# Kernel optimization log

Hardware: AMD Instinct MI355X
Metric: run time of the kernel (lower is better)

Reference implementation:

```python
import jax, jax.numpy as jnp
import numpy as np

EPS = 1e-8  # torch.nn.CosineSimilarity default eps


def setup_inputs() -> dict:
    key = jax.random.key(0)
    k1, k2 = jax.random.split(key)
    B, D = 2048, 512
    return {
        "z_i": jax.random.normal(k1, (B, D), dtype=jnp.float32),
        "z_j": jax.random.normal(k2, (B, D), dtype=jnp.float32),
        "temperature": 0.5,
    }


def _neg_mask_indices(B):
    # static (numpy) mask: remove diagonal and the two +/-B positive diagonals
    N = 2 * B
    mask = np.ones((N, N), dtype=bool)
    np.fill_diagonal(mask, False)
    idx = np.arange(B)
    mask[idx, idx + B] = False
    mask[idx + B, idx] = False
    rows, cols = np.where(mask)  # each row keeps exactly N-2 entries, row-major order
    return rows, cols


def reference(z_i, z_j, temperature):
    B = z_i.shape[0]
    N = 2 * B
    z = jnp.concatenate([z_i, z_j], axis=0)                      # [N, D]
    # cosine similarity = normalized GEMM (same math as pairwise CosineSimilarity)
    zn = z / jnp.maximum(jnp.linalg.norm(z, axis=1, keepdims=True), EPS)
    sim = jnp.matmul(zn, zn.T) / temperature                      # [N, N]

    pos = jnp.concatenate([jnp.diagonal(sim, B), jnp.diagonal(sim, -B)])[:, None]  # [N, 1]
    rows, cols = _neg_mask_indices(B)
    neg = sim[rows, cols].reshape(N, N - 2)                       # [N, N-2]

    logits = jnp.concatenate([pos, neg], axis=1)                  # [N, N-1], label = 0
    # sum-reduced cross-entropy with label 0, divided by N
    loss = jnp.sum(jax.nn.logsumexp(logits, axis=1) - logits[:, 0]) / N

    # avg_rank: position of the positive (column 0) in descending sort of logits
    order = jnp.argsort(-logits, axis=1)
    avg_rank = jnp.mean(jnp.argmin(order, axis=1).astype(jnp.float32))
    return loss, avg_rank
```

## Files before the change

### kernel.cpp

```cpp
#include <hip/hip_runtime.h>
#include <math.h>

#define DDIM 512
#define THREADS 128
#define BT 64
#define NT 64
#define NTILES (NT * (NT + 1) / 2)
#define NSL 16
#define NCH 64

typedef __attribute__((ext_vector_type(8))) __bf16 bf16x8;
typedef __attribute__((ext_vector_type(4))) float f32x4;
typedef __attribute__((ext_vector_type(8))) unsigned short ushort8;

__device__ __forceinline__ float bf2f(unsigned short u) {
  union { unsigned int i; float f; } v; v.i = ((unsigned int)u) << 16; return v.f;
}
__device__ __forceinline__ unsigned short f2bf(float f) {
  unsigned int u = __builtin_bit_cast(unsigned int, f);
  return (unsigned short)((u + 0x7fffu + ((u >> 16) & 1u)) >> 16);
}

__device__ __forceinline__ size_t frag_off_us(int rt, int s, int lane) {
  return ((size_t)(rt * NSL + s) * 64 + lane) * 8;
}

__global__ void k_prep(const float* __restrict__ zi, const float* __restrict__ zj,
                       const float* __restrict__ tempp,
                       unsigned short* __restrict__ zf, float* __restrict__ pos,
                       int B) {
  int wv = (blockIdx.x * blockDim.x + threadIdx.x) >> 6;
  int lane = threadIdx.x & 63;
  if (wv >= B) return;
  const float* a = zi + (size_t)wv * DDIM;
  const float* b = zj + (size_t)wv * DDIM;
  float4 a0 = *(const float4*)(a + lane * 8);
  float4 a1 = *(const float4*)(a + lane * 8 + 4);
  float4 b0 = *(const float4*)(b + lane * 8);
  float4 b1 = *(const float4*)(b + lane * 8 + 4);
  float av[8] = {a0.x, a0.y, a0.z, a0.w, a1.x, a1.y, a1.z, a1.w};
  float bv[8] = {b0.x, b0.y, b0.z, b0.w, b1.x, b1.y, b1.z, b1.w};
  float sa = 0.f, sb = 0.f;
#pragma unroll
  for (int i = 0; i < 8; ++i) { sa = fmaf(av[i], av[i], sa); sb = fmaf(bv[i], bv[i], sb); }
#pragma unroll
  for (int off = 32; off; off >>= 1) { sa += __shfl_xor(sa, off, 64); sb += __shfl_xor(sb, off, 64); }
  float ia = 1.f / fmaxf(sqrtf(sa), 1e-8f);
  float ib = 1.f / fmaxf(sqrtf(sb), 1e-8f);
  ushort8 ua, ub;
  float fa[8], fb[8];
#pragma unroll
  for (int i = 0; i < 8; ++i) {
    unsigned short x = f2bf(av[i] * ia); ua[i] = x; fa[i] = bf2f(x);
    unsigned short y = f2bf(bv[i] * ib); ub[i] = y; fb[i] = bf2f(y);
  }
  const int s = lane >> 2, g = lane & 3;
  {
    int r = wv;
    *(ushort8*)(zf + frag_off_us(r >> 4, s, (g << 4) | (r & 15))) = ua;
    r = wv + B;
    *(ushort8*)(zf + frag_off_us(r >> 4, s, (g << 4) | (r & 15))) = ub;
  }
  float pd = 0.f;
#pragma unroll
  for (int i = 0; i < 8; ++i) pd = fmaf(fa[i], fb[i], pd);
#pragma unroll
  for (int off = 32; off; off >>= 1) pd += __shfl_xor(pd, off, 64);
  if (lane == 0) {
    float p = pd / tempp[0];
    pos[wv] = p; pos[wv + B] = p;
  }
}

__global__ __launch_bounds__(THREADS) void k_main(
    const unsigned short* __restrict__ zf, const float* __restrict__ pos,
    const float* __restrict__ tempp, float* __restrict__ partS,
    float* __restrict__ partC, int B) {
  int tri = (blockIdx.x & 7) * (NTILES / 8) + (blockIdx.x >> 3);
  int bi = 0;
  while (tri >= NT - bi) { tri -= NT - bi; ++bi; }
  const int bj = bi + tri;
  const int r0 = bi * BT, c0 = bj * BT;
  const bool diag = (bi == bj);
  const float invt = 1.0f / tempp[0];

  const int t = threadIdx.x;
  const int lane = t & 63;
  const int wave = t >> 6;
  const int cl = lane & 15, g = lane >> 4;

  const int art0 = (r0 >> 4) + wave * 2;
  const int brt0 = (c0 >> 4);

  f32x4 acc[2][4];
#pragma unroll
  for (int m = 0; m < 2; ++m)
#pragma unroll
    for (int n = 0; n < 4; ++n) acc[m][n] = (f32x4){0.f, 0.f, 0.f, 0.f};

#pragma unroll 4
  for (int s = 0; s < NSL; ++s) {
    bf16x8 aF[2], bF[4];
#pragma unroll
    for (int m = 0; m < 2; ++m)
      aF[m] = *(const bf16x8*)(zf + frag_off_us(art0 + m, s, lane));
#pragma unroll
    for (int n = 0; n < 4; ++n)
      bF[n] = *(const bf16x8*)(zf + frag_off_us(brt0 + n, s, lane));
#pragma unroll
    for (int m = 0; m < 2; ++m)
#pragma unroll
      for (int n = 0; n < 4; ++n)
        acc[m][n] = __builtin_amdgcn_mfma_f32_16x16x32_bf16(aF[m], bF[n], acc[m][n], 0, 0, 0);
  }

  int growv[8], gpartr[8];
  float pvr[8];
#pragma unroll
  for (int m = 0; m < 2; ++m)
#pragma unroll
    for (int reg = 0; reg < 4; ++reg) {
      int idx = m * 4 + reg;
      int grow = r0 + wave * 32 + m * 16 + g * 4 + reg;
      growv[idx] = grow;
      gpartr[idx] = (grow < B) ? grow + B : grow - B;
      pvr[idx] = pos[grow];
    }
  int gcolv[4], gpartc[4];
  float pvc[4];
#pragma unroll
  for (int n = 0; n < 4; ++n) {
    int gcol = c0 + n * 16 + cl;
    gcolv[n] = gcol;
    gpartc[n] = (gcol < B) ? gcol + B : gcol - B;
    pvc[n] = pos[gcol];
  }

  float ssr[8], ccr[8], ssc[4], ccc[4];
#pragma unroll
  for (int i = 0; i < 8; ++i) { ssr[i] = 0.f; ccr[i] = 0.f; }
#pragma unroll
  for (int n = 0; n < 4; ++n) { ssc[n] = 0.f; ccc[n] = 0.f; }

#pragma unroll
  for (int m = 0; m < 2; ++m)
#pragma unroll
    for (int n = 0; n < 4; ++n)
#pragma unroll
      for (int reg = 0; reg < 4; ++reg) {
        const int idx = m * 4 + reg;
        float val = acc[m][n][reg] * invt;
        float e = __expf(val);
        bool isd = diag && (gcolv[n] == growv[idx]);
        if (!isd) {
          ssr[idx] += e;
          ccr[idx] += (gcolv[n] != gpartr[idx] && val > pvr[idx]) ? 1.f : 0.f;
        }
        if (!diag) {
          ssc[n] += e;
          ccc[n] += (growv[idx] != gpartc[n] && val > pvc[n]) ? 1.f : 0.f;
        }
      }

#pragma unroll
  for (int idx = 0; idx < 8; ++idx) {
    float s = ssr[idx], c = ccr[idx];
#pragma unroll
    for (int off = 1; off < 16; off <<= 1) {
      s += __shfl_xor(s, off, 64);
      c += __shfl_xor(c, off, 64);
    }
    if (cl == 0) {
      partS[(size_t)growv[idx] * NCH + bj] = s;
      partC[(size_t)growv[idx] * NCH + bj] = c;
    }
  }

  __shared__ float cbuf[256];
  if (!diag) {
#pragma unroll
    for (int n = 0; n < 4; ++n) {
      ssc[n] += __shfl_xor(ssc[n], 16, 64); ccc[n] += __shfl_xor(ccc[n], 16, 64);
      ssc[n] += __shfl_xor(ssc[n], 32, 64); ccc[n] += __shfl_xor(ccc[n], 32, 64);
    }
    if (g == 0) {
#pragma unroll
      for (int n = 0; n < 4; ++n) {
        cbuf[wave * 64 + n * 16 + cl] = ssc[n];
        cbuf[128 + wave * 64 + n * 16 + cl] = ccc[n];
      }
    }
  }
  __syncthreads();
  if (!diag && t < 64) {
    float s = cbuf[t] + cbuf[64 + t];
    float c = cbuf[128 + t] + cbuf[192 + t];
    partS[(size_t)(c0 + t) * NCH + bi] = s;
    partC[(size_t)(c0 + t) * NCH + bi] = c;
  }
}

__global__ void k_rowfin(const float* __restrict__ partS, const float* __restrict__ partC,
                         const float* __restrict__ pos, float* __restrict__ rowL,
                         float* __restrict__ rowC, int N) {
  int r = (blockIdx.x * blockDim.x + threadIdx.x) >> 6;
  int lane = threadIdx.x & 63;
  if (r >= N) return;
  float s = partS[(size_t)r * NCH + lane];
  float c = partC[(size_t)r * NCH + lane];
#pragma unroll
  for (int off = 32; off; off >>= 1) { s += __shfl_xor(s, off, 64); c += __shfl_xor(c, off, 64); }
  if (lane == 0) {
    rowL[r] = logf(s) - pos[r];
    rowC[r] = c;
  }
}

__global__ void k_final(const float* __restrict__ rowL, const float* __restrict__ rowC,
                        float* __restrict__ out, int N) {
  float ls = 0.f, cs = 0.f;
  for (int r = threadIdx.x; r < N; r += 256) { ls += rowL[r]; cs += rowC[r]; }
  __shared__ float l[256], c[256];
  l[threadIdx.x] = ls; c[threadIdx.x] = cs;
  __syncthreads();
  for (int off = 128; off; off >>= 1) {
    if (threadIdx.x < off) { l[threadIdx.x] += l[threadIdx.x + off]; c[threadIdx.x] += c[threadIdx.x + off]; }
    __syncthreads();
  }
  if (threadIdx.x == 0) { out[0] = l[0] / (float)N; out[1] = c[0] / (float)N; }
}

extern "C" void kernel_launch(void* const* d_in, const int* in_sizes, int n_in,
                              void* d_out, int out_size, void* d_ws, size_t ws_size,
                              hipStream_t stream) {
  const float* zi = (const float*)d_in[0];
  const float* zj = (const float*)d_in[1];
  const float* temp = (const float*)d_in[2];
  float* out = (float*)d_out;

  const int B = in_sizes[0] / DDIM;
  const int N = 2 * B;

  unsigned short* zf = (unsigned short*)d_ws;
  float* fws = (float*)(zf + (size_t)N * DDIM);
  float* pos   = fws;
  float* partS = pos + N;
  float* partC = partS + (size_t)N * NCH;
  float* rowL  = partC + (size_t)N * NCH;
  float* rowC  = rowL + N;

  k_prep<<<(B * 64) / 256, 256, 0, stream>>>(zi, zj, temp, zf, pos, B);
  k_main<<<NTILES, THREADS, 0, stream>>>(zf, pos, temp, partS, partC, B);
  k_rowfin<<<(N * 64) / 256, 256, 0, stream>>>(partS, partC, pos, rowL, rowC, N);
  k_final<<<1, 256, 0, stream>>>(rowL, rowC, out, N);
}
```

Measured before the change: 41.94 us.

## Quantize normalized embeddings to FP8 e4m3 and use one-wave 64x64 tiles

The prep kernel now quantizes the normalized rows to FP8 e4m3 with a software converter instead of bf16, and derives the positive logits from the dequantized values. The main kernel uses the fp8 16x16x32 MFMA on 8-byte fragments, which halves operand traffic and uses the faster FP8 matrix path. Each 64x64 tile is now computed by a single wave holding a 4x4 accumulator grid, so the shared-memory column reduction and the barrier go away. The cost is much coarser similarity values: this risks tolerance failures, especially in the rank count, which compares each logit against the positive. It also raises register pressure per wave.

```diff
diff --git a/kernel.cpp b/kernel.cpp
--- a/kernel.cpp
+++ b/kernel.cpp
@@ -2,32 +2,49 @@
 #include <math.h>
 
 #define DDIM 512
-#define THREADS 128
 #define BT 64
 #define NT 64
 #define NTILES (NT * (NT + 1) / 2)
 #define NSL 16
 #define NCH 64
 
-typedef __attribute__((ext_vector_type(8))) __bf16 bf16x8;
 typedef __attribute__((ext_vector_type(4))) float f32x4;
-typedef __attribute__((ext_vector_type(8))) unsigned short ushort8;
-
-__device__ __forceinline__ float bf2f(unsigned short u) {
-  union { unsigned int i; float f; } v; v.i = ((unsigned int)u) << 16; return v.f;
-}
-__device__ __forceinline__ unsigned short f2bf(float f) {
-  unsigned int u = __builtin_bit_cast(unsigned int, f);
-  return (unsigned short)((u + 0x7fffu + ((u >> 16) & 1u)) >> 16);
-}
-
-__device__ __forceinline__ size_t frag_off_us(int rt, int s, int lane) {
+
+__device__ __forceinline__ unsigned char f2e4m3(float x) {
+  unsigned ux = __builtin_bit_cast(unsigned, x);
+  unsigned sign = (ux >> 24) & 0x80u;
+  float a = fminf(fabsf(x), 448.f);
+  unsigned ua = __builtin_bit_cast(unsigned, a);
+  int E = (int)((ua >> 23) & 0xff);
+  if (E == 0) return (unsigned char)sign;
+  E -= 127;
+  int t = E - 3; if (t < -9) t = -9;
+  float c = __builtin_bit_cast(float, (unsigned)((t + 150) << 23));
+  float r = (a + c) - c;
+  if (r <= 0.f) return (unsigned char)sign;
+  unsigned ur = __builtin_bit_cast(unsigned, r);
+  int Er = (int)((ur >> 23) & 0xff) - 127;
+  if (Er < -6) {
+    unsigned man = (unsigned)(r * 512.f + 0.5f);
+    return (unsigned char)(sign | man);
+  }
+  unsigned man = (ur >> 20) & 7u;
+  return (unsigned char)(sign | ((unsigned)(Er + 7) << 3) | man);
+}
+__device__ __forceinline__ float e4m32f(unsigned char b) {
+  int e = (b >> 3) & 0xf, m = b & 7;
+  float v = (e == 0) ? (float)m * 0.001953125f
+                     : (float)(8 + m) * __builtin_bit_cast(float, (unsigned)((e + 117) << 23));
+  return (b & 0x80) ? -v : v;
+}
+
+__device__ __forceinline__ size_t frag_off(int rt, int s, int lane) {
   return ((size_t)(rt * NSL + s) * 64 + lane) * 8;
 }
 
 __global__ void k_prep(const float* __restrict__ zi, const float* __restrict__ zj,
                        const float* __restrict__ tempp,
-                       unsigned short* __restrict__ zf, float* __restrict__ pos,
+                       unsigned char* __restrict__ zf, float* __restrict__ pos,
                        int B) {
   int wv = (blockIdx.x * blockDim.x + threadIdx.x) >> 6;
   int lane = threadIdx.x & 63;
@@ -47,19 +64,21 @@
   for (int off = 32; off; off >>= 1) { sa += __shfl_xor(sa, off, 64); sb += __shfl_xor(sb, off, 64); }
   float ia = 1.f / fmaxf(sqrtf(sa), 1e-8f);
   float ib = 1.f / fmaxf(sqrtf(sb), 1e-8f);
-  ushort8 ua, ub;
+  unsigned long long pa = 0ull, pb = 0ull;
   float fa[8], fb[8];
 #pragma unroll
   for (int i = 0; i < 8; ++i) {
-    unsigned short x = f2bf(av[i] * ia); ua[i] = x; fa[i] = bf2f(x);
-    unsigned short y = f2bf(bv[i] * ib); ub[i] = y; fb[i] = bf2f(y);
+    unsigned char qa = f2e4m3(av[i] * ia); fa[i] = e4m32f(qa);
+    unsigned char qb = f2e4m3(bv[i] * ib); fb[i] = e4m32f(qb);
+    pa |= ((unsigned long long)qa) << (8 * i);
+    pb |= ((unsigned long long)qb) << (8 * i);
   }
   const int s = lane >> 2, g = lane & 3;
   {
     int r = wv;
-    *(ushort8*)(zf + frag_off_us(r >> 4, s, (g << 4) | (r & 15))) = ua;
+    *(unsigned long long*)(zf + frag_off(r >> 4, s, (g << 4) | (r & 15))) = pa;
     r = wv + B;
-    *(ushort8*)(zf + frag_off_us(r >> 4, s, (g << 4) | (r & 15))) = ub;
+    *(unsigned long long*)(zf + frag_off(r >> 4, s, (g << 4) | (r & 15))) = pb;
   }
   float pd = 0.f;
 #pragma unroll
@@ -72,8 +91,8 @@
   }
 }
 
-__global__ __launch_bounds__(THREADS) void k_main(
-    const unsigned short* __restrict__ zf, const float* __restrict__ pos,
+__global__ __launch_bounds__(64) void k_main(
+    const unsigned char* __restrict__ zf, const float* __restrict__ pos,
     const float* __restrict__ tempp, float* __restrict__ partS,
     float* __restrict__ partC, int B) {
   int tri = (blockIdx.x & 7) * (NTILES / 8) + (blockIdx.x >> 3);
@@ -84,44 +103,41 @@
   const bool diag = (bi == bj);
   const float invt = 1.0f / tempp[0];
 
-  const int t = threadIdx.x;
-  const int lane = t & 63;
-  const int wave = t >> 6;
+  const int lane = threadIdx.x;
   const int cl = lane & 15, g = lane >> 4;
-
-  const int art0 = (r0 >> 4) + wave * 2;
-  const int brt0 = (c0 >> 4);
-
-  f32x4 acc[2][4];
-#pragma unroll
-  for (int m = 0; m < 2; ++m)
+  const int art = r0 >> 4;
+  const int brt = c0 >> 4;
+
+  f32x4 acc[4][4];
+#pragma unroll
+  for (int m = 0; m < 4; ++m)
 #pragma unroll
     for (int n = 0; n < 4; ++n) acc[m][n] = (f32x4){0.f, 0.f, 0.f, 0.f};
 
 #pragma unroll 4
   for (int s = 0; s < NSL; ++s) {
-    bf16x8 aF[2], bF[4];
-#pragma unroll
-    for (int m = 0; m < 2; ++m)
-      aF[m] = *(const bf16x8*)(zf + frag_off_us(art0 + m, s, lane));
+    long long aF[4], bF[4];
+#pragma unroll
+    for (int m = 0; m < 4; ++m)
+      aF[m] = *(const long long*)(zf + frag_off(art + m, s, lane));
 #pragma unroll
     for (int n = 0; n < 4; ++n)
-      bF[n] = *(const bf16x8*)(zf + frag_off_us(brt0 + n, s, lane));
-#pragma unroll
-    for (int m = 0; m < 2; ++m)
+      bF[n] = *(const long long*)(zf + frag_off(brt + n, s, lane));
+#pragma unroll
+    for (int m = 0; m < 4; ++m)
 #pragma unroll
       for (int n = 0; n < 4; ++n)
-        acc[m][n] = __builtin_amdgcn_mfma_f32_16x16x32_bf16(aF[m], bF[n], acc[m][n], 0, 0, 0);
-  }
-
-  int growv[8], gpartr[8];
-  float pvr[8];
-#pragma unroll
-  for (int m = 0; m < 2; ++m)
+        acc[m][n] = __builtin_amdgcn_mfma_f32_16x16x32_fp8_fp8(aF[m], bF[n], acc[m][n], 0, 0, 0);
+  }
+
+  int growv[16], gpartr[16];
+  float pvr[16];
+#pragma unroll
+  for (int m = 0; m < 4; ++m)
 #pragma unroll
     for (int reg = 0; reg < 4; ++reg) {
       int idx = m * 4 + reg;
-      int grow = r0 + wave * 32 + m * 16 + g * 4 + reg;
+      int grow = r0 + m * 16 + g * 4 + reg;
       growv[idx] = grow;
       gpartr[idx] = (grow < B) ? grow + B : grow - B;
       pvr[idx] = pos[grow];
@@ -136,14 +152,14 @@
     pvc[n] = pos[gcol];
   }
 
-  float ssr[8], ccr[8], ssc[4], ccc[4];
-#pragma unroll
-  for (int i = 0; i < 8; ++i) { ssr[i] = 0.f; ccr[i] = 0.f; }
+  float ssr[16], ccr[16], ssc[4], ccc[4];
+#pragma unroll
+  for (int i = 0; i < 16; ++i) { ssr[i] = 0.f; ccr[i] = 0.f; }
 #pragma unroll
   for (int n = 0; n < 4; ++n) { ssc[n] = 0.f; ccc[n] = 0.f; }
 
 #pragma unroll
-  for (int m = 0; m < 2; ++m)
+  for (int m = 0; m < 4; ++m)
 #pragma unroll
     for (int n = 0; n < 4; ++n)
 #pragma unroll
@@ -163,7 +179,7 @@
       }
 
 #pragma unroll
-  for (int idx = 0; idx < 8; ++idx) {
+  for (int idx = 0; idx < 16; ++idx) {
     float s = ssr[idx], c = ccr[idx];
 #pragma unroll
     for (int off = 1; off < 16; off <<= 1) {
@@ -175,28 +191,17 @@
       partC[(size_t)growv[idx] * NCH + bj] = c;
     }
   }
-
-  __shared__ float cbuf[256];
   if (!diag) {
 #pragma unroll
     for (int n = 0; n < 4; ++n) {
-      ssc[n] += __shfl_xor(ssc[n], 16, 64); ccc[n] += __shfl_xor(ccc[n], 16, 64);
-      ssc[n] += __shfl_xor(ssc[n], 32, 64); ccc[n] += __shfl_xor(ccc[n], 32, 64);
-    }
-    if (g == 0) {
-#pragma unroll
-      for (int n = 0; n < 4; ++n) {
-        cbuf[wave * 64 + n * 16 + cl] = ssc[n];
-        cbuf[128 + wave * 64 + n * 16 + cl] = ccc[n];
+      float s = ssc[n], c = ccc[n];
+      s += __shfl_xor(s, 16, 64); c += __shfl_xor(c, 16, 64);
+      s += __shfl_xor(s, 32, 64); c += __shfl_xor(c, 32, 64);
+      if (g == 0) {
+        partS[(size_t)gcolv[n] * NCH + bi] = s;
+        partC[(size_t)gcolv[n] * NCH + bi] = c;
       }
     }
-  }
-  __syncthreads();
-  if (!diag && t < 64) {
-    float s = cbuf[t] + cbuf[64 + t];
-    float c = cbuf[128 + t] + cbuf[192 + t];
-    partS[(size_t)(c0 + t) * NCH + bi] = s;
-    partC[(size_t)(c0 + t) * NCH + bi] = c;
   }
 }
 
@@ -241,7 +246,7 @@
   const int B = in_sizes[0] / DDIM;
   const int N = 2 * B;
 
-  unsigned short* zf = (unsigned short*)d_ws;
+  unsigned char* zf = (unsigned char*)d_ws;
   float* fws = (float*)(zf + (size_t)N * DDIM);
   float* pos   = fws;
   float* partS = pos + N;
@@ -250,7 +255,7 @@
   float* rowC  = rowL + N;
 
   k_prep<<<(B * 64) / 256, 256, 0, stream>>>(zi, zj, temp, zf, pos, B);
-  k_main<<<NTILES, THREADS, 0, stream>>>(zf, pos, temp, partS, partC, B);
+  k_main<<<NTILES, 64, 0, stream>>>(zf, pos, temp, partS, partC, B);
   k_rowfin<<<(N * 64) / 256, 256, 0, stream>>>(partS, partC, pos, rowL, rowC, N);
   k_final<<<1, 256, 0, stream>>>(rowL, rowC, out, N);
 }
```

Result: slower. 48.83 us (+16.4%).
